# Kernel optimization log

Hardware: AMD Instinct MI355X
Metric: run time of the kernel (lower is better)

## Reference

```python
import math
import jax, jax.numpy as jnp
import numpy as np

B, S, HID = 1, 2048, 2048
H, D = 32, 64            # heads, head_dim = HID // H
THETA = 10000.0
EPS = 1e-6
LAYER_IDX = 12
LAM_INIT = 0.8 - 0.6 * math.exp(-0.3 * LAYER_IDX)  # lambda_init_fn(layer_idx)
SCALE = 1.0 / math.sqrt(D)


def _rope_cos_sin(seq_len, dim):
    inv_freq = 1.0 / (THETA ** (np.arange(0, dim, 2, dtype=np.float64) / dim))
    freqs = np.outer(np.arange(seq_len, dtype=np.float64), inv_freq)
    emb = np.concatenate([freqs, freqs], axis=-1)  # [S, D] (llama duplicates freqs)
    return jnp.asarray(np.cos(emb), jnp.float32), jnp.asarray(np.sin(emb), jnp.float32)


def _rotate_half(x):
    return jnp.concatenate([-x[..., D // 2:], x[..., : D // 2]], axis=-1)


def _apply_rope(x, cos, sin):
    # x: [B, H, S, D]; cos/sin: [S, D] broadcast over B, H
    return x * cos + _rotate_half(x) * sin


def setup_inputs() -> dict:
    key = jax.random.key(0)
    ks = jax.random.split(key, 10)
    return {
        "hidden_states": jax.random.normal(ks[0], (B, S, HID), jnp.float32),
        "Wq": jax.random.normal(ks[1], (2 * HID, HID), jnp.float32) * 0.02,
        "Wk": jax.random.normal(ks[2], (2 * HID, HID), jnp.float32) * 0.02,
        "Wv": jax.random.normal(ks[3], (HID, HID), jnp.float32) * 0.02,
        "Wo": jax.random.normal(ks[4], (HID, HID), jnp.float32) * 0.02,
        "lambda_q1": jax.random.normal(ks[5], (D,), jnp.float32) * 0.1,
        "lambda_k1": jax.random.normal(ks[6], (D,), jnp.float32) * 0.1,
        "lambda_q2": jax.random.normal(ks[7], (D,), jnp.float32) * 0.1,
        "lambda_k2": jax.random.normal(ks[8], (D,), jnp.float32) * 0.1,
        "subln_w": jnp.ones((D,), jnp.float32),
    }


def reference(hidden_states, Wq, Wk, Wv, Wo,
              lambda_q1, lambda_k1, lambda_q2, lambda_k2, subln_w):
    # Projections (nn.Linear, no bias): x @ W.T
    q = hidden_states @ Wq.T                       # [B, S, 2*HID]
    k = hidden_states @ Wk.T                       # [B, S, 2*HID]
    v = hidden_states @ Wv.T                       # [B, S, HID]

    def to_heads(t):  # [B, S, H*D] -> [B, H, S, D]
        return t.reshape(B, S, H, D).transpose(0, 2, 1, 3)

    q1, q2 = jnp.split(q, 2, axis=-1)
    k1, k2 = jnp.split(k, 2, axis=-1)
    q1, q2, k1, k2, v = map(to_heads, (q1, q2, k1, k2, v))

    cos, sin = _rope_cos_sin(S, D)
    q1, k1 = _apply_rope(q1, cos, sin), _apply_rope(k1, cos, sin)
    q2, k2 = _apply_rope(q2, cos, sin), _apply_rope(k2, cos, sin)

    # Causal additive mask [S, S]
    causal = jnp.tril(jnp.ones((S, S), bool))
    neg_inf = jnp.finfo(jnp.float32).min
    mask = jnp.where(causal, 0.0, neg_inf)

    s1 = jnp.einsum("bhqd,bhkd->bhqk", q1, k1) * SCALE + mask
    s2 = jnp.einsum("bhqd,bhkd->bhqk", q2, k2) * SCALE + mask

    lam = (jnp.exp(jnp.sum(lambda_q1 * lambda_k1))
           - jnp.exp(jnp.sum(lambda_q2 * lambda_k2)) + LAM_INIT)

    attn_w = jax.nn.softmax(s1, axis=-1) - lam * jax.nn.softmax(s2, axis=-1)
    attn = jnp.einsum("bhqk,bhkd->bhqd", attn_w, v)  # [B, H, S, D]

    # Head-wise RMSNorm (LlamaRMSNorm over value_head_dim)
    var = jnp.mean(jnp.square(attn), axis=-1, keepdims=True)
    attn = attn * jax.lax.rsqrt(var + EPS) * subln_w
    attn = attn * (1.0 - LAM_INIT)

    out = attn.transpose(0, 2, 1, 3).reshape(B, S, HID) @ Wo.T
    return out
```

## Files before the change

kernel.cpp:

```cpp
#include <hip/hip_runtime.h>


typedef __bf16 bf16;
typedef __bf16 bf16x4 __attribute__((ext_vector_type(4)));
typedef __bf16 bf16x8 __attribute__((ext_vector_type(8)));
typedef float  f32x4  __attribute__((ext_vector_type(4)));
typedef unsigned int u32;
typedef u32 u32x2 __attribute__((ext_vector_type(2)));
typedef u32 u32x4 __attribute__((ext_vector_type(4)));

#define MFMA(a, b, c) __builtin_amdgcn_mfma_f32_16x16x32_bf16((a), (b), (c), 0, 0, 0)

#define S_LEN   2048
#define HID_DIM 2048
#define NHEAD   32
#define HD      64
#define QKV_N   10240
#define LAM_INIT 0.7836057665316245f
#define ONE_MINUS_LAM_INIT 0.21639423346837553f
#define QSCALE  0.18033688011112042f
#define RMS_EPS 1e-6f
#define L2T     0.4152410118609203f

__device__ __forceinline__ void gld16(const void* g, void* l) {
    __builtin_amdgcn_global_load_lds(
        (const __attribute__((address_space(1))) void*)g,
        (__attribute__((address_space(3))) void*)l, 16, 0, 0);
}

__device__ __forceinline__ void pa_build(u32 x, u32 y, int quad, u32& wlo, u32& whi) {
#if __has_builtin(__builtin_amdgcn_permlane32_swap) && __has_builtin(__builtin_amdgcn_permlane16_swap)
    u32x2 s = __builtin_amdgcn_permlane32_swap(x, y, false, false);
    u32x2 t = __builtin_amdgcn_permlane16_swap(s.x, s.y, false, false);
    wlo = t.x;
    whi = t.y;
#else
    const u32 x16 = (u32)__shfl_xor((int)x, 16, 64);
    const u32 x32 = (u32)__shfl_xor((int)x, 32, 64);
    const u32 x48 = (u32)__shfl_xor((int)x, 48, 64);
    const u32 y16 = (u32)__shfl_xor((int)y, 16, 64);
    const u32 y32 = (u32)__shfl_xor((int)y, 32, 64);
    const u32 y48 = (u32)__shfl_xor((int)y, 48, 64);
    wlo = (quad == 0) ? x   : (quad == 1) ? x48 : (quad == 2) ? y32 : y16;
    whi = (quad == 0) ? x16 : (quad == 1) ? x32 : (quad == 2) ? y48 : y;
#endif
}

__global__ void cvt_all(const float* __restrict__ hs, const float* __restrict__ Wq,
                        const float* __restrict__ Wk, const float* __restrict__ Wv,
                        const float* __restrict__ Wo,
                        const float* __restrict__ lq1, const float* __restrict__ lk1,
                        const float* __restrict__ lq2, const float* __restrict__ lk2,
                        bf16* __restrict__ hsb, bf16* __restrict__ Wb,
                        bf16* __restrict__ Wob, float* __restrict__ lam_out) {
    const int bid = blockIdx.x;
    if (bid >= 7168) {
        const int t = threadIdx.x;
        if (t < 64) {
            float a = lq1[t] * lk1[t];
            float b = lq2[t] * lk2[t];
            #pragma unroll
            for (int off = 32; off > 0; off >>= 1) {
                a += __shfl_xor(a, off, 64);
                b += __shfl_xor(b, off, 64);
            }
            if (t == 0) lam_out[0] = expf(a) - expf(b) + LAM_INIT;
        }
        return;
    }
    const float* src; bf16* dst; int off;
    if      (bid < 1024) { src = hs; dst = hsb;            off = bid;        }
    else if (bid < 3072) { src = Wq; dst = Wb;             off = bid - 1024; }
    else if (bid < 5120) { src = Wk; dst = Wb +  8388608;  off = bid - 3072; }
    else if (bid < 6144) { src = Wv; dst = Wb + 16777216;  off = bid - 5120; }
    else                 { src = Wo; dst = Wob;            off = bid - 6144; }
    const int i = off * 4096 + threadIdx.x * 16;
    float4 a = *(const float4*)(src + i);
    float4 b = *(const float4*)(src + i + 4);
    float4 c = *(const float4*)(src + i + 8);
    float4 d = *(const float4*)(src + i + 12);
    bf16x8 o0 = { (bf16)a.x, (bf16)a.y, (bf16)a.z, (bf16)a.w,
                  (bf16)b.x, (bf16)b.y, (bf16)b.z, (bf16)b.w };
    bf16x8 o1 = { (bf16)c.x, (bf16)c.y, (bf16)c.z, (bf16)c.w,
                  (bf16)d.x, (bf16)d.y, (bf16)d.z, (bf16)d.w };
    *(bf16x8*)(dst + i)     = o0;
    *(bf16x8*)(dst + i + 8) = o1;
}

__global__ __launch_bounds__(256, 3)
void qkv_rope_gemm(const bf16* __restrict__ A, const bf16* __restrict__ B,
                   bf16* __restrict__ Q1, bf16* __restrict__ Q2,
                   bf16* __restrict__ K1, bf16* __restrict__ K2,
                   bf16* __restrict__ Vt) {
    __shared__ __align__(16) bf16 As[128 * 64];
    __shared__ __align__(16) bf16 Bs[128 * 64];
    const int tid  = threadIdx.x;
    const int wave = tid >> 6, lane = tid & 63;
    const int wm = wave >> 1, wn = wave & 1;
    const int l = lane & 15, quad = lane >> 4;
    const int m0 = blockIdx.y * 128, n0 = blockIdx.x * 128;

    f32x4 acc[4][4];
    #pragma unroll
    for (int i = 0; i < 4; ++i)
        #pragma unroll
        for (int j = 0; j < 4; ++j) acc[i][j] = (f32x4){0.f, 0.f, 0.f, 0.f};

    const int rr  = tid >> 3;
    const int csw = ((tid & 7) ^ (rr & 7)) * 8;
    const bf16* Ag = A + (size_t)(m0 + rr) * HID_DIM + csw;
    const bf16* Bg = B + (size_t)(n0 + rr) * HID_DIM + csw;

    for (int kt = 0; kt < HID_DIM; kt += 64) {
        __syncthreads();
        #pragma unroll
        for (int j = 0; j < 4; ++j) {
            gld16(Ag + (size_t)(32 * j) * HID_DIM + kt, As + j * 2048 + tid * 8);
            gld16(Bg + (size_t)(32 * j) * HID_DIM + kt, Bs + j * 2048 + tid * 8);
        }
        __syncthreads();

        #pragma unroll
        for (int ks = 0; ks < 2; ++ks) {
            const int co = (((ks << 2) | quad) ^ (l & 7)) << 3;
            bf16x8 hf[4], wf[4];
            #pragma unroll
            for (int hi = 0; hi < 4; ++hi)
                hf[hi] = *(const bf16x8*)(As + (wm * 64 + hi * 16 + l) * 64 + co);
            #pragma unroll
            for (int wi = 0; wi < 4; ++wi)
                wf[wi] = *(const bf16x8*)(Bs + (wn * 64 + wi * 16 + l) * 64 + co);
            #pragma unroll
            for (int wi = 0; wi < 4; ++wi)
                #pragma unroll
                for (int hi = 0; hi < 4; ++hi)
                    acc[wi][hi] = MFMA(wf[wi], hf[hi], acc[wi][hi]);
        }
    }

    const int c = n0 + wn * 64;
    const int sbase = m0 + wm * 64;
    bf16* dst; int off; float scale = 1.0f; bool isv = false;
    if      (c < 2048) { dst = Q1; off = c;        scale = QSCALE; }
    else if (c < 4096) { dst = Q2; off = c - 2048; scale = QSCALE; }
    else if (c < 6144) { dst = K1; off = c - 4096; }
    else if (c < 8192) { dst = K2; off = c - 6144; }
    else               { isv = true; off = c - 8192; }
    const int h = off >> 6;

    if (!isv) {
        float invf[2][4];
        #pragma unroll
        for (int p = 0; p < 2; ++p)
            #pragma unroll
            for (int r = 0; r < 4; ++r)
                invf[p][r] = exp2f(-(float)(p * 16 + quad * 4 + r) * L2T);

        #pragma unroll
        for (int hi = 0; hi < 4; ++hi) {
            const float s = (float)(sbase + hi * 16 + l);
            float cs[2][4], sn[2][4];
            #pragma unroll
            for (int p = 0; p < 2; ++p)
                #pragma unroll
                for (int r = 0; r < 4; ++r) {
                    const float ang = s * invf[p][r];
                    cs[p][r] = __cosf(ang);
                    sn[p][r] = __sinf(ang);
                }
            bf16* rowp = dst + ((size_t)h * S_LEN + sbase + hi * 16 + l) * HD + quad * 4;
            #pragma unroll
            for (int wi = 0; wi < 4; ++wi) {
                const int p = wi & 1;
                const float sign = (wi < 2) ? -1.0f : 1.0f;
                bf16x4 o;
                #pragma unroll
                for (int r = 0; r < 4; ++r)
                    o[r] = (bf16)((acc[wi][hi][r] * cs[p][r] +
                                   sign * acc[wi ^ 2][hi][r] * sn[p][r]) * scale);
                *(bf16x4*)(rowp + wi * 16) = o;
            }
        }
    } else {
        #pragma unroll
        for (int wi = 0; wi < 4; ++wi)
            #pragma unroll
            for (int r = 0; r < 4; ++r) {
                bf16* vrow = Vt + ((size_t)h * HD + wi * 16 + quad * 4 + r) * S_LEN + sbase;
                #pragma unroll
                for (int hi = 0; hi < 4; ++hi)
                    vrow[hi * 16 + l] = (bf16)acc[wi][hi][r];
            }
    }
}

__global__ __launch_bounds__(256, 3)
void gemm_bt(const bf16* __restrict__ A, const bf16* __restrict__ B,
             float* __restrict__ C, int M, int N, int K) {
    __shared__ __align__(16) bf16 As[128 * 64];
    __shared__ __align__(16) bf16 Bs[64 * 64];
    const int tid  = threadIdx.x;
    const int wave = tid >> 6, lane = tid & 63;
    const int wm = wave >> 1, wn = wave & 1;
    const int l = lane & 15, quad = lane >> 4;
    const int m0 = blockIdx.y * 128, n0 = blockIdx.x * 64;

    f32x4 acc[4][2];
    #pragma unroll
    for (int i = 0; i < 4; ++i)
        #pragma unroll
        for (int j = 0; j < 2; ++j) acc[i][j] = (f32x4){0.f, 0.f, 0.f, 0.f};

    const int rr  = tid >> 3;
    const int csw = ((tid & 7) ^ (rr & 7)) * 8;
    const bf16* Ag = A + (size_t)(m0 + rr) * K + csw;
    const bf16* Bg = B + (size_t)(n0 + rr) * K + csw;

    for (int kt = 0; kt < K; kt += 64) {
        __syncthreads();
        #pragma unroll
        for (int jj = 0; jj < 4; ++jj)
            gld16(Ag + (size_t)(32 * jj) * K + kt, As + jj * 2048 + tid * 8);
        #pragma unroll
        for (int jj = 0; jj < 2; ++jj)
            gld16(Bg + (size_t)(32 * jj) * K + kt, Bs + jj * 2048 + tid * 8);
        __syncthreads();

        #pragma unroll
        for (int ks = 0; ks < 2; ++ks) {
            const int co = (((ks << 2) | quad) ^ (l & 7)) << 3;
            bf16x8 af[4], bfr[2];
            #pragma unroll
            for (int mi = 0; mi < 4; ++mi)
                af[mi] = *(const bf16x8*)(As + (wm * 64 + mi * 16 + l) * 64 + co);
            #pragma unroll
            for (int ni = 0; ni < 2; ++ni)
                bfr[ni] = *(const bf16x8*)(Bs + (wn * 32 + ni * 16 + l) * 64 + co);
            #pragma unroll
            for (int mi = 0; mi < 4; ++mi)
                #pragma unroll
                for (int ni = 0; ni < 2; ++ni)
                    acc[mi][ni] = MFMA(af[mi], bfr[ni], acc[mi][ni]);
        }
    }

    #pragma unroll
    for (int mi = 0; mi < 4; ++mi)
        #pragma unroll
        for (int ni = 0; ni < 2; ++ni)
            #pragma unroll
            for (int r = 0; r < 4; ++r) {
                const int row = m0 + wm * 64 + mi * 16 + quad * 4 + r;
                const int col = n0 + wn * 32 + ni * 16 + l;
                C[(size_t)row * N + col] = acc[mi][ni][r];
            }
}

#define ATTN_CORE(DIAGF)                                                      \
    {                                                                         \
        _Pragma("unroll")                                                     \
        for (int g = 0; g < 4; ++g) {                                         \
            f32x4 c[2];                                                       \
            _Pragma("unroll")                                                 \
            for (int mk = 0; mk < 2; ++mk) {                                  \
                c[mk] = (f32x4){0.f, 0.f, 0.f, 0.f};                          \
                c[mk] = MFMA(ka[mk][0], qf[g][0], c[mk]);                     \
                c[mk] = MFMA(ka[mk][1], qf[g][1], c[mk]);                     \
            }                                                                 \
            u32 dw[2][2];                                                     \
            float lsum = 0.f;                                                 \
            _Pragma("unroll")                                                 \
            for (int mk = 0; mk < 2; ++mk) {                                  \
                float p[4];                                                   \
                _Pragma("unroll")                                             \
                for (int r = 0; r < 4; ++r) {                                 \
                    p[r] = __builtin_amdgcn_exp2f(c[mk][r]);                  \
                    if (DIAGF && ((2 * ks + mk) * 16 + quad * 4 + r > g * 16 + l)) \
                        p[r] = 0.f;                                           \
                    lsum += p[r];                                             \
                }                                                             \
                asm("v_cvt_pk_bf16_f32 %0, %1, %2" : "=v"(dw[mk][0]) : "v"(p[0]), "v"(p[1])); \
                asm("v_cvt_pk_bf16_f32 %0, %1, %2" : "=v"(dw[mk][1]) : "v"(p[2]), "v"(p[3])); \
            }                                                                 \
            csum[g] += lsum;                                                  \
            u32 w0, w1, w2, w3;                                               \
            pa_build(dw[0][0], dw[1][0], quad, w0, w2);                       \
            pa_build(dw[0][1], dw[1][1], quad, w1, w3);                       \
            u32x4 wv = {w0, w1, w2, w3};                                      \
            bf16x8 pa;                                                        \
            __builtin_memcpy(&pa, &wv, 16);                                   \
            _Pragma("unroll")                                                 \
            for (int nd = 0; nd < 4; ++nd)                                    \
                O[g][nd] = MFMA(pa, vb[nd], O[g][nd]);                        \
        }                                                                     \
    }

__global__ __launch_bounds__(512, 2)
void diff_attn(const bf16* __restrict__ Q1, const bf16* __restrict__ K1,
               const bf16* __restrict__ Q2, const bf16* __restrict__ K2,
               const bf16* __restrict__ Vt, const float* __restrict__ lam_p,
               const float* __restrict__ subln_w, bf16* __restrict__ attn_out) {
    const int bid  = blockIdx.x;
    const int h    = bid & 31;
    const int pp   = bid >> 5;
    const int tid  = threadIdx.x;
    const int wave = tid >> 6, lane = tid & 63;
    const int qhalf = wave >> 2, sid = (wave >> 1) & 1, ks = wave & 1;
    const int l = lane & 15, quad = lane >> 4;

    __shared__ __align__(16) char smem[98304];

    const bf16* K1g = K1 + (size_t)h * S_LEN * HD;
    const bf16* K2g = K2 + (size_t)h * S_LEN * HD;
    const bf16* Vtg = Vt + (size_t)h * HD * S_LEN;
    const bf16* Qv  = (sid ? Q2 : Q1) + (size_t)h * S_LEN * HD;

    const int rr  = tid >> 3;
    const int csw = ((tid & 7) ^ (rr & 7)) * 8;
    const int sw8 = l & 7;

    auto stage = [&](int kv, int bufb) {
        #pragma unroll
        for (int s = 0; s < 2; ++s) {
            gld16(K1g + (size_t)(kv + s * 64 + rr) * HD + csw,
                  (bf16*)(smem + bufb)         + s * 4096 + tid * 8);
            gld16(K2g + (size_t)(kv + s * 64 + rr) * HD + csw,
                  (bf16*)(smem + bufb + 16384) + s * 4096 + tid * 8);
            gld16(Vtg + (size_t)rr * S_LEN + kv + s * 64 + csw,
                  (bf16*)(smem + bufb + 32768) + s * 4096 + tid * 8);
        }
    };

    for (int it = 0; it < 2; ++it) {
        const int qb = it ? pp : (15 - pp);
        const int q0 = qb * 128;
        const bf16* Qh = Qv + (size_t)(q0 + qhalf * 64) * HD;

        bf16x8 qf[4][2];
        #pragma unroll
        for (int g = 0; g < 4; ++g)
            #pragma unroll
            for (int dh = 0; dh < 2; ++dh)
                qf[g][dh] = *(const bf16x8*)(Qh + (g * 16 + l) * HD + dh * 32 + quad * 8);

        f32x4 O[4][4];
        #pragma unroll
        for (int g = 0; g < 4; ++g)
            #pragma unroll
            for (int nd = 0; nd < 4; ++nd)
                O[g][nd] = (f32x4){0.f, 0.f, 0.f, 0.f};
        float csum[4] = {0.f, 0.f, 0.f, 0.f};

        const int nt = qb + 1;
        const int tq = 2 * qb + qhalf;

        stage(0, 0);
        asm volatile("s_waitcnt vmcnt(0)" ::: "memory");
        __builtin_amdgcn_s_barrier();

        for (int tt = 0; tt < nt; ++tt) {
            const int bb = (tt & 1) * 49152;
            if (tt + 1 < nt) stage((tt + 1) * 128, 49152 - bb);

            #pragma unroll
            for (int sub = 0; sub < 2; ++sub) {
                const int t64 = 2 * tt + sub;
                if (t64 <= tq) {
                    const bf16* Ksm = (const bf16*)(smem + bb + (sid ? 16384 : 0))
                                      + sub * 4096;
                    const bf16* Vts = (const bf16*)(smem + bb + 32768) + sub * 4096;

                    bf16x8 ka[2][2];
                    #pragma unroll
                    for (int mk = 0; mk < 2; ++mk) {
                        const int krow = ((2 * ks + mk) * 16 + l) * 64;
                        ka[mk][0] = *(const bf16x8*)(Ksm + krow + ((quad ^ sw8) << 3));
                        ka[mk][1] = *(const bf16x8*)(Ksm + krow + (((4 + quad) ^ sw8) << 3));
                    }
                    bf16x8 vb[4];
                    #pragma unroll
                    for (int nd = 0; nd < 4; ++nd)
                        vb[nd] = *(const bf16x8*)(Vts + (nd * 16 + l) * 64 +
                                                  ((((ks << 2) + quad) ^ sw8) << 3));

                    __builtin_amdgcn_s_setprio(1);
                    if (t64 == tq) {
                        ATTN_CORE(1)
                    } else {
                        ATTN_CORE(0)
                    }
                    __builtin_amdgcn_s_setprio(0);
                }
            }

            asm volatile("s_waitcnt vmcnt(0)" ::: "memory");
            __builtin_amdgcn_s_barrier();
        }

        __syncthreads();
        #pragma unroll
        for (int round = 0; round < 2; ++round) {
            float* dO = (float*)(smem + sid * 17408);
            float* dC = (float*)(smem + 34816 + sid * 1024);
            if (qhalf == round && ks == 1) {
                #pragma unroll
                for (int g = 0; g < 4; ++g)
                    #pragma unroll
                    for (int nd = 0; nd < 4; ++nd)
                        *(f32x4*)(dO + lane * 68 + (g * 4 + nd) * 4) = O[g][nd];
                #pragma unroll
                for (int g = 0; g < 4; ++g) dC[g * 64 + lane] = csum[g];
            }
            __syncthreads();
            if (qhalf == round && ks == 0) {
                #pragma unroll
                for (int g = 0; g < 4; ++g) {
                    #pragma unroll
                    for (int nd = 0; nd < 4; ++nd)
                        O[g][nd] += *(const f32x4*)(dO + lane * 68 + (g * 4 + nd) * 4);
                    csum[g] += dC[g * 64 + lane];
                }
            }
            __syncthreads();
        }

        #pragma unroll
        for (int g = 0; g < 4; ++g) {
            csum[g] += __shfl_xor(csum[g], 16, 64);
            csum[g] += __shfl_xor(csum[g], 32, 64);
        }

        float* epi = (float*)smem;

        if (sid == 1 && ks == 0) {
            const float lam = lam_p[0];
            #pragma unroll
            for (int mi = 0; mi < 4; ++mi)
                #pragma unroll
                for (int r = 0; r < 4; ++r) {
                    const float inv = lam / __shfl(csum[mi], quad * 4 + r, 64);
                    const int row = qhalf * 64 + mi * 16 + quad * 4 + r;
                    #pragma unroll
                    for (int ni = 0; ni < 4; ++ni)
                        epi[row * 65 + ni * 16 + l] = O[mi][ni][r] * inv;
                }
        }
        __syncthreads();

        if (sid == 0 && ks == 0) {
            float sw[4];
            #pragma unroll
            for (int ni = 0; ni < 4; ++ni) sw[ni] = subln_w[ni * 16 + l];

            #pragma unroll
            for (int mi = 0; mi < 4; ++mi) {
                float inv1[4];
                #pragma unroll
                for (int r = 0; r < 4; ++r)
                    inv1[r] = 1.0f / __shfl(csum[mi], quad * 4 + r, 64);

                float v[4][4]; float ssq[4] = {0.f, 0.f, 0.f, 0.f};
                #pragma unroll
                for (int ni = 0; ni < 4; ++ni)
                    #pragma unroll
                    for (int r = 0; r < 4; ++r) {
                        const int row = qhalf * 64 + mi * 16 + quad * 4 + r;
                        const float x = O[mi][ni][r] * inv1[r] - epi[row * 65 + ni * 16 + l];
                        v[ni][r] = x;
                        ssq[r] += x * x;
                    }
                #pragma unroll
                for (int r = 0; r < 4; ++r) {
                    float s = ssq[r];
                    s += __shfl_xor(s, 1, 64);
                    s += __shfl_xor(s, 2, 64);
                    s += __shfl_xor(s, 4, 64);
                    s += __shfl_xor(s, 8, 64);
                    ssq[r] = rsqrtf(s * (1.0f / 64.0f) + RMS_EPS) * ONE_MINUS_LAM_INIT;
                }
                #pragma unroll
                for (int ni = 0; ni < 4; ++ni)
                    #pragma unroll
                    for (int r = 0; r < 4; ++r) {
                        const int row = q0 + qhalf * 64 + mi * 16 + quad * 4 + r;
                        attn_out[(size_t)row * HID_DIM + h * 64 + ni * 16 + l] =
                            (bf16)(v[ni][r] * ssq[r] * sw[ni]);
                    }
            }
        }
        __syncthreads();
    }
}

extern "C" void kernel_launch(void* const* d_in, const int* in_sizes, int n_in,
                              void* d_out, int out_size, void* d_ws, size_t ws_size,
                              hipStream_t stream) {
    const float* hs  = (const float*)d_in[0];
    const float* Wq  = (const float*)d_in[1];
    const float* Wk  = (const float*)d_in[2];
    const float* Wv  = (const float*)d_in[3];
    const float* Wo  = (const float*)d_in[4];
    const float* lq1 = (const float*)d_in[5];
    const float* lk1 = (const float*)d_in[6];
    const float* lq2 = (const float*)d_in[7];
    const float* lk2 = (const float*)d_in[8];
    const float* slw = (const float*)d_in[9];

    if (ws_size < 151000000u) return;

    char* ws = (char*)d_ws;
    bf16*  hsb  = (bf16*)(ws);
    bf16*  Wb   = (bf16*)(ws + 8388608);
    bf16*  Wob  = (bf16*)(ws + 50331648);
    bf16*  Q1b  = (bf16*)(ws + 100663296);
    bf16*  K1b  = (bf16*)(ws + 109051904);
    bf16*  Q2b  = (bf16*)(ws + 117440512);
    bf16*  K2b  = (bf16*)(ws + 125829120);
    bf16*  Vtb  = (bf16*)(ws + 134217728);
    bf16*  abuf = (bf16*)(ws + 142606336);
    float* lamp = (float*)(ws + 150994944);

    cvt_all<<<7169, 256, 0, stream>>>(hs, Wq, Wk, Wv, Wo, lq1, lk1, lq2, lk2,
                                      hsb, Wb, Wob, lamp);

    qkv_rope_gemm<<<dim3(QKV_N / 128, S_LEN / 128), 256, 0, stream>>>(
        hsb, Wb, Q1b, Q2b, K1b, K2b, Vtb);

    diff_attn<<<256, 512, 0, stream>>>(Q1b, K1b, Q2b, K2b, Vtb, lamp, slw, abuf);

    gemm_bt<<<dim3(32, 16), 256, 0, stream>>>(
        abuf, Wob, (float*)d_out, S_LEN, HID_DIM, HID_DIM);
}
```

Before: 344.2 us.

## Process paired long and short query blocks in one shared KV sweep

Instead of two sequential passes over K/V tiles (one for the long query block 15-pp and one for the short block pp), the kernel now keeps both blocks' Q fragments and accumulators in registers. It streams the K/V tiles once, applying the short block's work only on tiles up to its causal limit. This removes the duplicated global-to-LDS staging and barriers for the short block's prefix. The cost is doubled accumulator and Q register state, which raises register pressure and may cause spills or reduce occupancy under launch_bounds(512,2).

```diff
diff --git a/kernel.cpp b/kernel.cpp
--- a/kernel.cpp
+++ b/kernel.cpp
@@ -256,7 +256,7 @@
             }
 }
 
-#define ATTN_CORE(DIAGF)                                                      \
+#define ATTN_CORE(O, CS, QF, DIAGF)                                           \
     {                                                                         \
         _Pragma("unroll")                                                     \
         for (int g = 0; g < 4; ++g) {                                         \
@@ -264,8 +264,8 @@
             _Pragma("unroll")                                                 \
             for (int mk = 0; mk < 2; ++mk) {                                  \
                 c[mk] = (f32x4){0.f, 0.f, 0.f, 0.f};                          \
-                c[mk] = MFMA(ka[mk][0], qf[g][0], c[mk]);                     \
-                c[mk] = MFMA(ka[mk][1], qf[g][1], c[mk]);                     \
+                c[mk] = MFMA(ka[mk][0], QF[g][0], c[mk]);                     \
+                c[mk] = MFMA(ka[mk][1], QF[g][1], c[mk]);                     \
             }                                                                 \
             u32 dw[2][2];                                                     \
             float lsum = 0.f;                                                 \
@@ -282,7 +282,7 @@
                 asm("v_cvt_pk_bf16_f32 %0, %1, %2" : "=v"(dw[mk][0]) : "v"(p[0]), "v"(p[1])); \
                 asm("v_cvt_pk_bf16_f32 %0, %1, %2" : "=v"(dw[mk][1]) : "v"(p[2]), "v"(p[3])); \
             }                                                                 \
-            csum[g] += lsum;                                                  \
+            CS[g] += lsum;                                                    \
             u32 w0, w1, w2, w3;                                               \
             pa_build(dw[0][0], dw[1][0], quad, w0, w2);                       \
             pa_build(dw[0][1], dw[1][1], quad, w1, w3);                       \
@@ -331,72 +331,91 @@
         }
     };
 
-    for (int it = 0; it < 2; ++it) {
-        const int qb = it ? pp : (15 - pp);
-        const int q0 = qb * 128;
-        const bf16* Qh = Qv + (size_t)(q0 + qhalf * 64) * HD;
-
-        bf16x8 qf[4][2];
+    const int qbL = 15 - pp, qbS = pp;
+    const int q0L = qbL * 128, q0S = qbS * 128;
+    const int tqL = 2 * qbL + qhalf;
+    const int tqS = 2 * qbS + qhalf;
+
+    bf16x8 qfL[4][2], qfS[4][2];
+    {
+        const bf16* QhL = Qv + (size_t)(q0L + qhalf * 64) * HD;
+        const bf16* QhS = Qv + (size_t)(q0S + qhalf * 64) * HD;
         #pragma unroll
         for (int g = 0; g < 4; ++g)
             #pragma unroll
-            for (int dh = 0; dh < 2; ++dh)
-                qf[g][dh] = *(const bf16x8*)(Qh + (g * 16 + l) * HD + dh * 32 + quad * 8);
-
-        f32x4 O[4][4];
-        #pragma unroll
-        for (int g = 0; g < 4; ++g)
-            #pragma unroll
-            for (int nd = 0; nd < 4; ++nd)
-                O[g][nd] = (f32x4){0.f, 0.f, 0.f, 0.f};
-        float csum[4] = {0.f, 0.f, 0.f, 0.f};
-
-        const int nt = qb + 1;
-        const int tq = 2 * qb + qhalf;
-
-        stage(0, 0);
+            for (int dh = 0; dh < 2; ++dh) {
+                qfL[g][dh] = *(const bf16x8*)(QhL + (g * 16 + l) * HD + dh * 32 + quad * 8);
+                qfS[g][dh] = *(const bf16x8*)(QhS + (g * 16 + l) * HD + dh * 32 + quad * 8);
+            }
+    }
+
+    f32x4 OL[4][4], OS[4][4];
+    #pragma unroll
+    for (int g = 0; g < 4; ++g)
+        #pragma unroll
+        for (int nd = 0; nd < 4; ++nd) {
+            OL[g][nd] = (f32x4){0.f, 0.f, 0.f, 0.f};
+            OS[g][nd] = (f32x4){0.f, 0.f, 0.f, 0.f};
+        }
+    float csL[4] = {0.f, 0.f, 0.f, 0.f};
+    float csS[4] = {0.f, 0.f, 0.f, 0.f};
+
+    const int nt = qbL + 1;
+
+    stage(0, 0);
+    asm volatile("s_waitcnt vmcnt(0)" ::: "memory");
+    __builtin_amdgcn_s_barrier();
+
+    for (int tt = 0; tt < nt; ++tt) {
+        const int bb = (tt & 1) * 49152;
+        if (tt + 1 < nt) stage((tt + 1) * 128, 49152 - bb);
+
+        #pragma unroll
+        for (int sub = 0; sub < 2; ++sub) {
+            const int t64 = 2 * tt + sub;
+            if (t64 <= tqL) {
+                const bf16* Ksm = (const bf16*)(smem + bb + (sid ? 16384 : 0))
+                                  + sub * 4096;
+                const bf16* Vts = (const bf16*)(smem + bb + 32768) + sub * 4096;
+
+                bf16x8 ka[2][2];
+                #pragma unroll
+                for (int mk = 0; mk < 2; ++mk) {
+                    const int krow = ((2 * ks + mk) * 16 + l) * 64;
+                    ka[mk][0] = *(const bf16x8*)(Ksm + krow + ((quad ^ sw8) << 3));
+                    ka[mk][1] = *(const bf16x8*)(Ksm + krow + (((4 + quad) ^ sw8) << 3));
+                }
+                bf16x8 vb[4];
+                #pragma unroll
+                for (int nd = 0; nd < 4; ++nd)
+                    vb[nd] = *(const bf16x8*)(Vts + (nd * 16 + l) * 64 +
+                                              ((((ks << 2) + quad) ^ sw8) << 3));
+
+                __builtin_amdgcn_s_setprio(1);
+                if (t64 == tqL) {
+                    ATTN_CORE(OL, csL, qfL, 1)
+                } else {
+                    ATTN_CORE(OL, csL, qfL, 0)
+                }
+                if (t64 < tqS) {
+                    ATTN_CORE(OS, csS, qfS, 0)
+                } else if (t64 == tqS) {
+                    ATTN_CORE(OS, csS, qfS, 1)
+                }
+                __builtin_amdgcn_s_setprio(0);
+            }
+        }
+
         asm volatile("s_waitcnt vmcnt(0)" ::: "memory");
         __builtin_amdgcn_s_barrier();
-
-        for (int tt = 0; tt < nt; ++tt) {
-            const int bb = (tt & 1) * 49152;
-            if (tt + 1 < nt) stage((tt + 1) * 128, 49152 - bb);
-
-            #pragma unroll
-            for (int sub = 0; sub < 2; ++sub) {
-                const int t64 = 2 * tt + sub;
-                if (t64 <= tq) {
-                    const bf16* Ksm = (const bf16*)(smem + bb + (sid ? 16384 : 0))
-                                      + sub * 4096;
-                    const bf16* Vts = (const bf16*)(smem + bb + 32768) + sub * 4096;
-
-                    bf16x8 ka[2][2];
-                    #pragma unroll
-                    for (int mk = 0; mk < 2; ++mk) {
-                        const int krow = ((2 * ks + mk) * 16 + l) * 64;
-                        ka[mk][0] = *(const bf16x8*)(Ksm + krow + ((quad ^ sw8) << 3));
-                        ka[mk][1] = *(const bf16x8*)(Ksm + krow + (((4 + quad) ^ sw8) << 3));
-                    }
-                    bf16x8 vb[4];
-                    #pragma unroll
-                    for (int nd = 0; nd < 4; ++nd)
-                        vb[nd] = *(const bf16x8*)(Vts + (nd * 16 + l) * 64 +
-                                                  ((((ks << 2) + quad) ^ sw8) << 3));
-
-                    __builtin_amdgcn_s_setprio(1);
-                    if (t64 == tq) {
-                        ATTN_CORE(1)
-                    } else {
-                        ATTN_CORE(0)
-                    }
-                    __builtin_amdgcn_s_setprio(0);
-                }
-            }
-
-            asm volatile("s_waitcnt vmcnt(0)" ::: "memory");
-            __builtin_amdgcn_s_barrier();
-        }
-
+    }
+
+    const float lam = lam_p[0];
+    float sw[4];
+    #pragma unroll
+    for (int ni = 0; ni < 4; ++ni) sw[ni] = subln_w[ni * 16 + l];
+
+    auto finish = [&](f32x4 (&O)[4][4], float (&csum)[4], int q0) {
         __syncthreads();
         #pragma unroll
         for (int round = 0; round < 2; ++round) {
@@ -433,7 +452,6 @@
         float* epi = (float*)smem;
 
         if (sid == 1 && ks == 0) {
-            const float lam = lam_p[0];
             #pragma unroll
             for (int mi = 0; mi < 4; ++mi)
                 #pragma unroll
@@ -448,10 +466,6 @@
         __syncthreads();
 
         if (sid == 0 && ks == 0) {
-            float sw[4];
-            #pragma unroll
-            for (int ni = 0; ni < 4; ++ni) sw[ni] = subln_w[ni * 16 + l];
-
             #pragma unroll
             for (int mi = 0; mi < 4; ++mi) {
                 float inv1[4];
@@ -489,7 +503,10 @@
             }
         }
         __syncthreads();
-    }
+    };
+
+    finish(OS, csS, q0S);
+    finish(OL, csL, q0L);
 }
 
 extern "C" void kernel_launch(void* const* d_in, const int* in_sizes, int n_in,
```

Result: slower. 372.0 us (+8.1%).
